# Kernel optimization log

Hardware: AMD Instinct MI355X
Metric: run time of the kernel (lower is better)

## Reference

```python
import jax, jax.numpy as jnp
import numpy as np

SCORE_THRESH = 0.5
NMS_THRESH = 0.4
TOP_K = 1000  # fixed pre-NMS candidate budget (jit-safe replacement for boolean masking)
STRIDES = (8, 16, 32)
H, W = 2176, 3840


def _anchor_centers(fh, fw, stride):
    yv, xv = jnp.meshgrid(jnp.arange(fh), jnp.arange(fw), indexing='ij')
    return (jnp.stack([xv, yv], -1).reshape(-1, 2).astype(jnp.float32)) * stride  # [N,2]


def _decode_level(scores, bbox, kps, stride):
    fh, fw = H // stride, W // stride
    c = _anchor_centers(fh, fw, stride)                 # [N,2]
    s = jax.nn.sigmoid(scores.reshape(-1))              # [N]
    d = bbox.reshape(-1, 4) * stride                    # [N,4]
    boxes = jnp.concatenate([c - d[:, :2], c + d[:, 2:4]], axis=1)  # x1y1x2y2
    k = kps.reshape(-1, 5, 2) * stride + c[:, None, :]  # (x,y) pairs
    return s, boxes, k.reshape(-1, 10)


def _iou_matrix(b):
    area = (b[:, 2] - b[:, 0]) * (b[:, 3] - b[:, 1])
    lt = jnp.maximum(b[:, None, :2], b[None, :, :2])
    rb = jnp.minimum(b[:, None, 2:], b[None, :, 2:])
    wh = jnp.clip(rb - lt, 0.0)
    inter = wh[..., 0] * wh[..., 1]
    return inter / jnp.clip(area[:, None] + area[None, :] - inter, 1e-9)


def _nms_keep(iou, valid):
    n = iou.shape[0]
    ar = jnp.arange(n)

    def body(i, keep):
        sup = (iou[i] > NMS_THRESH) & (ar > i) & keep[i]
        return keep & ~sup

    return jax.lax.fori_loop(0, n, body, valid)


def reference(x, scores8, bbox8, kps8, scores16, bbox16, kps16, scores32, bbox32, kps32):
    levels = ((scores8, bbox8, kps8), (scores16, bbox16, kps16), (scores32, bbox32, kps32))
    ss, bs, ks = [], [], []
    for (s, b, k), stride in zip(levels, STRIDES):
        si, bi, ki = _decode_level(s, b, k, stride)
        ss.append(si); bs.append(bi); ks.append(ki)
    scores = jnp.concatenate(ss)   # [N_total]
    boxes = jnp.concatenate(bs)    # [N_total,4]
    kpss = jnp.concatenate(ks)     # [N_total,10]

    masked = jnp.where(scores > SCORE_THRESH, scores, -1.0)
    top_s, idx = jax.lax.top_k(masked, TOP_K)
    valid = top_s > SCORE_THRESH
    b = boxes[idx]
    k = kpss[idx]

    keep = jax.lax.stop_gradient(_nms_keep(_iou_matrix(b), valid))
    final_boxes = jnp.where(keep[:, None], b, 0.0)
    final_scores = jnp.where(keep, top_s, 0.0)
    final_kpss = jnp.where(keep[:, None], k, 0.0)
    return final_boxes, final_scores, final_kpss


def setup_inputs() -> dict:
    key = jax.random.key(0)
    ks = jax.random.split(key, 10)
    n8 = (H // 8) * (W // 8)
    n16 = (H // 16) * (W // 16)
    n32 = (H // 32) * (W // 32)
    return {
        'x': jax.random.normal(ks[0], (1, 3, H, W), jnp.float32),
        'scores8': jax.random.normal(ks[1], (1, n8, 1), jnp.float32),
        'bbox8': jax.random.uniform(ks[2], (1, n8, 4), jnp.float32),
        'kps8': jax.random.normal(ks[3], (1, n8, 10), jnp.float32),
        'scores16': jax.random.normal(ks[4], (1, n16, 1), jnp.float32),
        'bbox16': jax.random.uniform(ks[5], (1, n16, 4), jnp.float32),
        'kps16': jax.random.normal(ks[6], (1, n16, 10), jnp.float32),
        'scores32': jax.random.normal(ks[7], (1, n32, 1), jnp.float32),
        'bbox32': jax.random.uniform(ks[8], (1, n32, 4), jnp.float32),
        'kps32': jax.random.normal(ks[9], (1, n32, 10), jnp.float32),
    }
```

## Files before the change

### kernel.cpp

```cpp
#include <hip/hip_runtime.h>
#include <stdint.h>

typedef unsigned int u32;
typedef unsigned long long u64;

#define N8   130560
#define N16  32640
#define N32  8160
#define NTOT 171360
#define NTOT4 42840
#define TOPK 1000
#define NWORDS 16
#define NBINS 4096
#define NREP 4
#define BUCKET_SCALE 682.0f
#define LIST_CAP 2048
#define NBLK 168
#define IOU_TASKS (TOPK * NWORDS)
#define IOU_BLKS 63
#define NMS_CACHE 256

#define OFF_HIST 0
#define OFF_META 65536
#define OFF_NZ   65792
#define MEMSET_BYTES 65920
#define OFF_LIST 65920
#define OFF_MASK 82304

__device__ __forceinline__ u64 ald64(const u64* p) {
  return __hip_atomic_load(p, __ATOMIC_RELAXED, __HIP_MEMORY_SCOPE_AGENT);
}
__device__ __forceinline__ void ast64(u64* p, u64 v) {
  __hip_atomic_store(p, v, __ATOMIC_RELAXED, __HIP_MEMORY_SCOPE_AGENT);
}

__device__ __forceinline__ u32 bucket_of(float x) {
  u32 b = (u32)(x * BUCKET_SCALE);
  return b > (NBINS - 1) ? (NBINS - 1) : b;
}

__device__ __forceinline__ float4 load_logit4(int v, const float* s8, const float* s16,
                                              const float* s32) {
  int e = v * 4;
  if (e < N8) return ((const float4*)s8)[v];
  if (e < N8 + N16) return ((const float4*)s16)[v - N8 / 4];
  return ((const float4*)s32)[v - (N8 + N16) / 4];
}

__device__ __forceinline__ bool iou_gt04(float4 a, float4 b) {
#pragma clang fp contract(off)
  float areaA = (a.z - a.x) * (a.w - a.y);
  float areaB = (b.z - b.x) * (b.w - b.y);
  float ltx = fmaxf(a.x, b.x);
  float lty = fmaxf(a.y, b.y);
  float rbx = fminf(a.z, b.z);
  float rby = fminf(a.w, b.w);
  float wx = rbx - ltx; wx = wx > 0.0f ? wx : 0.0f;
  float wy = rby - lty; wy = wy > 0.0f ? wy : 0.0f;
  float inter = wx * wy;
  float un = areaA + areaB - inter;
  un = un > 1e-9f ? un : 1e-9f;
  return (inter / un) > 0.4f;
}

__device__ __forceinline__ u64 valid_word(int w, u32 vcnt) {
  int lo = w * 64;
  if ((int)vcnt >= lo + 64) return ~0ull;
  if ((int)vcnt <= lo) return 0ull;
  return (1ull << (vcnt - (u32)lo)) - 1ull;
}

__global__ void __launch_bounds__(256) k_hist(
    const float* __restrict__ s8, const float* __restrict__ s16, const float* __restrict__ s32,
    u32* __restrict__ hist) {
  int v = blockIdx.x * 256 + threadIdx.x;
  if (v >= NTOT4) return;
  u32* h = hist + (blockIdx.x & (NREP - 1)) * NBINS;
  float4 x = load_logit4(v, s8, s16, s32);
  if (x.x > 0.0f) atomicAdd(&h[bucket_of(x.x)], 1u);
  if (x.y > 0.0f) atomicAdd(&h[bucket_of(x.y)], 1u);
  if (x.z > 0.0f) atomicAdd(&h[bucket_of(x.z)], 1u);
  if (x.w > 0.0f) atomicAdd(&h[bucket_of(x.w)], 1u);
}

__global__ void __launch_bounds__(256) k_findB_compact(
    const float* __restrict__ s8, const float* __restrict__ s16, const float* __restrict__ s32,
    const u32* __restrict__ hist, u32* __restrict__ meta, u64* __restrict__ list) {
  __shared__ u32 hloc[NBINS];
  __shared__ u32 csum[256];
  __shared__ u32 sB;
  int t = threadIdx.x;
#pragma unroll
  for (int k = 0; k < 16; ++k) {
    int b = k * 256 + t;
    u32 v = 0;
#pragma unroll
    for (int r = 0; r < NREP; ++r) v += hist[r * NBINS + b];
    hloc[b] = v;
  }
  __syncthreads();
  u32 sum = 0;
  int base = t * 16;
#pragma unroll
  for (int k = 0; k < 16; ++k) sum += hloc[base + k];
  csum[t] = sum;
  __syncthreads();
  for (int off = 1; off < 256; off <<= 1) {
    u32 add = (t + off < 256) ? csum[t + off] : 0u;
    __syncthreads();
    csum[t] += add;
    __syncthreads();
  }
  if (t == 0 && csum[0] < TOPK) sB = 0;
  u32 above = (t < 255) ? csum[t + 1] : 0u;
  if (csum[t] >= TOPK && above < TOPK) {
    u32 cum = above, Bv = (u32)(t * 16);
    for (int b = t * 16 + 15; b >= t * 16; --b) {
      cum += hloc[b];
      if (cum >= TOPK) { Bv = (u32)b; break; }
    }
    sB = Bv;
  }
  __syncthreads();
  const u32 B = sB;

  int v = blockIdx.x * 256 + t;
  if (v >= NTOT4) return;
  float4 x = load_logit4(v, s8, s16, s32);
  float c[4] = {x.x, x.y, x.z, x.w};
#pragma unroll
  for (int j = 0; j < 4; ++j) {
    float xx = c[j];
    if (xx > 0.0f && bucket_of(xx) >= B) {
      u32 pos = atomicAdd(&meta[1], 1u);
      if (pos < LIST_CAP) {
        u32 idx = (u32)(v * 4 + j);
        list[pos] = ((u64)__float_as_uint(xx) << 32) | (u64)(~idx);
      }
    }
  }
}

__global__ void __launch_bounds__(256) k_rank_decode(
    const u64* __restrict__ list, const u32* __restrict__ meta,
    const float* __restrict__ bb8,  const float* __restrict__ kp8,
    const float* __restrict__ bb16, const float* __restrict__ kp16,
    const float* __restrict__ bb32, const float* __restrict__ kp32,
    float* __restrict__ out) {
  __shared__ u64 keys[LIST_CAP];
  int t = threadIdx.x;
  u32 cnt = meta[1];
  if (cnt > LIST_CAP) cnt = LIST_CAP;
  for (int j = t; j < LIST_CAP; j += 256) keys[j] = (j < (int)cnt) ? list[j] : 0ull;
  __syncthreads();
  int tid = blockIdx.x * 256 + t;
  if (tid < (int)cnt) {
    u64 my = keys[tid];
    int rank = 0, j = 0;
    for (; j + 4 <= (int)cnt; j += 4)
      rank += (keys[j] > my) + (keys[j + 1] > my) + (keys[j + 2] > my) + (keys[j + 3] > my);
    for (; j < (int)cnt; ++j) rank += (keys[j] > my);
    if (rank < TOPK) {
      float lx = __uint_as_float((u32)(my >> 32));
      float sc = (float)(1.0 / (1.0 + exp(-(double)lx)));
      u32 idx = ~((u32)my);
      float4 box;
      float kv[10];
      int p, xq, yq;
      float st;
      const float *bb, *kp;
      if (idx < N8) {
        st = 8.f;  p = (int)idx;              xq = p % 480; yq = p / 480; bb = bb8;  kp = kp8;
      } else if (idx < N8 + N16) {
        st = 16.f; p = (int)idx - N8;         xq = p % 240; yq = p / 240; bb = bb16; kp = kp16;
      } else {
        st = 32.f; p = (int)idx - (N8 + N16); xq = p % 120; yq = p / 120; bb = bb32; kp = kp32;
      }
      float cx = (float)xq * st, cy = (float)yq * st;
      {
#pragma clang fp contract(off)
        float d0 = bb[4 * p + 0] * st;
        float d1 = bb[4 * p + 1] * st;
        float d2 = bb[4 * p + 2] * st;
        float d3 = bb[4 * p + 3] * st;
        box.x = cx - d0; box.y = cy - d1; box.z = cx + d2; box.w = cy + d3;
        for (int q = 0; q < 10; ++q)
          kv[q] = kp[10 * p + q] * st + ((q & 1) ? cy : cx);
      }
      ((float4*)out)[rank] = box;
      out[4000 + rank] = sc;
      for (int q = 0; q < 10; ++q) out[5000 + 10 * rank + q] = kv[q];
    }
  } else if (tid < TOPK) {
    ((float4*)out)[tid] = make_float4(0.f, 0.f, 0.f, 0.f);
    out[4000 + tid] = 0.f;
    for (int q = 0; q < 10; ++q) out[5000 + 10 * tid + q] = 0.f;
  }
}

__global__ void __launch_bounds__(256) k_iou_nms(
    const u32* __restrict__ meta_ro, u32* meta, u64* nzWords, u64* mask, float* out) {
  __shared__ __align__(16) char smem[36864];
  __shared__ int isLast;
  __shared__ u32 sPc[16], sOff17[17];
  __shared__ u64 sRem[NWORDS];
  int t = threadIdx.x;
  int blk = blockIdx.x;

  float4* boxes = (float4*)smem;
  for (int r = t; r < TOPK; r += 256) boxes[r] = ((const float4*)out)[r];
  __syncthreads();
  int task = blk * 256 + t;
  if (task < IOU_TASKS) {
    int w = task / 1000;
    int i = task - w * 1000;
    float4 a = boxes[i];
    int bse = w * 64;
    int jend = (bse + 64) < TOPK ? (bse + 64) : TOPK;
    u64 bits = 0;
    for (int j = bse; j < jend; ++j)
      if (j > i && iou_gt04(a, boxes[j])) bits |= 1ull << (j - bse);
    ast64(&mask[(u64)w * 1000 + i], bits);
    if (bits) atomicOr(&nzWords[i >> 6], 1ull << (i & 63));
  }
  __syncthreads();
  if (t == 0)
    isLast = (__hip_atomic_fetch_add(&meta[56], 1u, __ATOMIC_RELAXED,
                                     __HIP_MEMORY_SCOPE_AGENT) == (u32)(IOU_BLKS - 1));
  __syncthreads();
  if (!isLast) return;

  u32 cnt = meta_ro[1];
  if (cnt > LIST_CAP) cnt = LIST_CAP;
  const u32 vcnt = cnt < TOPK ? cnt : TOPK;
  u32* rows = (u32*)smem;
  u64* cache = (u64*)(smem + 4096);
  u64 nzv = 0;
  if (t < NWORDS) {
    nzv = ald64(&nzWords[t]) & valid_word(t, vcnt);
    sPc[t] = (u32)__popcll(nzv);
  }
  __syncthreads();
  if (t == 0) {
    u32 o = 0;
    for (int w = 0; w < NWORDS; ++w) { sOff17[w] = o; o += sPc[w]; }
    sOff17[16] = o;
  }
  __syncthreads();
  if (t < NWORDS) {
    u64 m = nzv;
    u32 o = sOff17[t];
    while (m) { int b = __builtin_ctzll(m); m &= m - 1; rows[o++] = (u32)(t * 64 + b); }
  }
  __syncthreads();
  const int S = (int)sOff17[16];
  const int Sc = S < NMS_CACHE ? S : NMS_CACHE;
  for (int idx = t; idx < Sc * NWORDS; idx += 256) {
    int s = idx >> 4, w = idx & 15;
    cache[s * NWORDS + w] = ald64(&mask[(u64)w * 1000 + rows[s]]);
  }
  __syncthreads();
  if (t < 64) {
    u64 remv = 0;
    for (int s = 0; s < S; ++s) {
      u32 row = rows[s];
      int c = (int)(row >> 6), b = (int)(row & 63);
      u64 remc = __shfl(remv, c);
      if (!((remc >> b) & 1ull)) {
        u64 m = 0;
        if (t < NWORDS)
          m = (s < NMS_CACHE) ? cache[s * NWORDS + t] : ald64(&mask[(u64)t * 1000 + row]);
        remv |= m;
      }
    }
    if (t < NWORDS) sRem[t] = valid_word(t, vcnt) & remv;
  }
  __syncthreads();
  for (int r = t; r < TOPK; r += 256) {
    if ((sRem[r >> 6] >> (r & 63)) & 1ull) {
      ((float4*)out)[r] = make_float4(0.f, 0.f, 0.f, 0.f);
      out[4000 + r] = 0.f;
      for (int q = 0; q < 10; ++q) out[5000 + 10 * r + q] = 0.f;
    }
  }
}

extern "C" void kernel_launch(void* const* d_in, const int* in_sizes, int n_in,
                              void* d_out, int out_size, void* d_ws, size_t ws_size,
                              hipStream_t stream) {
  const float* s8   = (const float*)d_in[1];
  const float* bb8  = (const float*)d_in[2];
  const float* kp8  = (const float*)d_in[3];
  const float* s16  = (const float*)d_in[4];
  const float* bb16 = (const float*)d_in[5];
  const float* kp16 = (const float*)d_in[6];
  const float* s32  = (const float*)d_in[7];
  const float* bb32 = (const float*)d_in[8];
  const float* kp32 = (const float*)d_in[9];

  char* ws = (char*)d_ws;
  u32* hist    = (u32*)(ws + OFF_HIST);
  u32* meta    = (u32*)(ws + OFF_META);
  u64* nzWords = (u64*)(ws + OFF_NZ);
  u64* list    = (u64*)(ws + OFF_LIST);
  u64* mask    = (u64*)(ws + OFF_MASK);
  float* out   = (float*)d_out;

  hipMemsetAsync(ws, 0, MEMSET_BYTES, stream);
  k_hist<<<NBLK, 256, 0, stream>>>(s8, s16, s32, hist);
  k_findB_compact<<<NBLK, 256, 0, stream>>>(s8, s16, s32, hist, meta, list);
  k_rank_decode<<<8, 256, 0, stream>>>(list, meta, bb8, kp8, bb16, kp16, bb32, kp32, out);
  k_iou_nms<<<IOU_BLKS, 256, 0, stream>>>(meta, meta, nzWords, mask, out);
}
```

Baseline: 205.5 us.

## Fuse threshold search, compaction and rank-decode into one kernel with grid-level spin sync

Removes the memset and merges the bin-threshold search, candidate compaction and rank/decode stages into a single kernel. Blocks coordinate through global atomic counters and spin-waits. The histogram now uses per-block shared-memory atomics and writes per-block partials, which are reduced in parallel across 32 blocks. Rank/decode is spread over 32 blocks of 64 active threads instead of 8 blocks. The aim is to cut launch and memset overhead and global atomic contention. In exchange it relies on all 168 blocks being co-resident and adds a larger partial-histogram write and read.

```diff
diff --git a/kernel.cpp b/kernel.cpp
--- a/kernel.cpp
+++ b/kernel.cpp
@@ -12,23 +12,30 @@
 #define TOPK 1000
 #define NWORDS 16
 #define NBINS 4096
-#define NREP 4
 #define BUCKET_SCALE 682.0f
 #define LIST_CAP 2048
 #define NBLK 168
+#define NRED 32
+#define RANK_BLKS 32
 #define IOU_TASKS (TOPK * NWORDS)
 #define IOU_BLKS 63
 #define NMS_CACHE 256
 
-#define OFF_HIST 0
-#define OFF_META 65536
-#define OFF_NZ   65792
-#define MEMSET_BYTES 65920
-#define OFF_LIST 65920
-#define OFF_MASK 82304
-
+#define OFF_PART 0
+#define OFF_RED  2752512
+#define OFF_META 2768896
+#define OFF_NZ   2769152
+#define OFF_LIST 2769280
+#define OFF_MASK 2785664
+
+__device__ __forceinline__ u32 ald32(const u32* p) {
+  return __hip_atomic_load(p, __ATOMIC_RELAXED, __HIP_MEMORY_SCOPE_AGENT);
+}
 __device__ __forceinline__ u64 ald64(const u64* p) {
   return __hip_atomic_load(p, __ATOMIC_RELAXED, __HIP_MEMORY_SCOPE_AGENT);
+}
+__device__ __forceinline__ void ast32(u32* p, u32 v) {
+  __hip_atomic_store(p, v, __ATOMIC_RELAXED, __HIP_MEMORY_SCOPE_AGENT);
 }
 __device__ __forceinline__ void ast64(u64* p, u64 v) {
   __hip_atomic_store(p, v, __ATOMIC_RELAXED, __HIP_MEMORY_SCOPE_AGENT);
@@ -72,88 +79,130 @@
 
 __global__ void __launch_bounds__(256) k_hist(
     const float* __restrict__ s8, const float* __restrict__ s16, const float* __restrict__ s32,
-    u32* __restrict__ hist) {
-  int v = blockIdx.x * 256 + threadIdx.x;
-  if (v >= NTOT4) return;
-  u32* h = hist + (blockIdx.x & (NREP - 1)) * NBINS;
-  float4 x = load_logit4(v, s8, s16, s32);
-  if (x.x > 0.0f) atomicAdd(&h[bucket_of(x.x)], 1u);
-  if (x.y > 0.0f) atomicAdd(&h[bucket_of(x.y)], 1u);
-  if (x.z > 0.0f) atomicAdd(&h[bucket_of(x.z)], 1u);
-  if (x.w > 0.0f) atomicAdd(&h[bucket_of(x.w)], 1u);
-}
-
-__global__ void __launch_bounds__(256) k_findB_compact(
+    u32* __restrict__ part, u32* __restrict__ meta, u64* __restrict__ nzWords) {
+  __shared__ u32 lh[NBINS];
+  int t = threadIdx.x, blk = blockIdx.x;
+#pragma unroll
+  for (int k = 0; k < 16; ++k) lh[k * 256 + t] = 0;
+  __syncthreads();
+  int v = blk * 256 + t;
+  if (v < NTOT4) {
+    float4 x = load_logit4(v, s8, s16, s32);
+    if (x.x > 0.0f) atomicAdd(&lh[bucket_of(x.x)], 1u);
+    if (x.y > 0.0f) atomicAdd(&lh[bucket_of(x.y)], 1u);
+    if (x.z > 0.0f) atomicAdd(&lh[bucket_of(x.z)], 1u);
+    if (x.w > 0.0f) atomicAdd(&lh[bucket_of(x.w)], 1u);
+  }
+  __syncthreads();
+#pragma unroll
+  for (int k = 0; k < 16; ++k) part[blk * NBINS + k * 256 + t] = lh[k * 256 + t];
+  if (blk == 0) {
+    if (t < 64) meta[t] = 0;
+    if (t < NWORDS) nzWords[t] = 0ull;
+  }
+}
+
+__global__ void __launch_bounds__(256) k_sel(
     const float* __restrict__ s8, const float* __restrict__ s16, const float* __restrict__ s32,
-    const u32* __restrict__ hist, u32* __restrict__ meta, u64* __restrict__ list) {
-  __shared__ u32 hloc[NBINS];
-  __shared__ u32 csum[256];
-  __shared__ u32 sB;
-  int t = threadIdx.x;
-#pragma unroll
-  for (int k = 0; k < 16; ++k) {
-    int b = k * 256 + t;
-    u32 v = 0;
-#pragma unroll
-    for (int r = 0; r < NREP; ++r) v += hist[r * NBINS + b];
-    hloc[b] = v;
-  }
-  __syncthreads();
-  u32 sum = 0;
-  int base = t * 16;
-#pragma unroll
-  for (int k = 0; k < 16; ++k) sum += hloc[base + k];
-  csum[t] = sum;
-  __syncthreads();
-  for (int off = 1; off < 256; off <<= 1) {
-    u32 add = (t + off < 256) ? csum[t + off] : 0u;
-    __syncthreads();
-    csum[t] += add;
-    __syncthreads();
-  }
-  if (t == 0 && csum[0] < TOPK) sB = 0;
-  u32 above = (t < 255) ? csum[t + 1] : 0u;
-  if (csum[t] >= TOPK && above < TOPK) {
-    u32 cum = above, Bv = (u32)(t * 16);
-    for (int b = t * 16 + 15; b >= t * 16; --b) {
-      cum += hloc[b];
-      if (cum >= TOPK) { Bv = (u32)b; break; }
-    }
-    sB = Bv;
-  }
-  __syncthreads();
-  const u32 B = sB;
-
-  int v = blockIdx.x * 256 + t;
-  if (v >= NTOT4) return;
-  float4 x = load_logit4(v, s8, s16, s32);
-  float c[4] = {x.x, x.y, x.z, x.w};
-#pragma unroll
-  for (int j = 0; j < 4; ++j) {
-    float xx = c[j];
-    if (xx > 0.0f && bucket_of(xx) >= B) {
-      u32 pos = atomicAdd(&meta[1], 1u);
-      if (pos < LIST_CAP) {
-        u32 idx = (u32)(v * 4 + j);
-        list[pos] = ((u64)__float_as_uint(xx) << 32) | (u64)(~idx);
-      }
-    }
-  }
-}
-
-__global__ void __launch_bounds__(256) k_rank_decode(
-    const u64* __restrict__ list, const u32* __restrict__ meta,
     const float* __restrict__ bb8,  const float* __restrict__ kp8,
     const float* __restrict__ bb16, const float* __restrict__ kp16,
     const float* __restrict__ bb32, const float* __restrict__ kp32,
+    const u32* __restrict__ part, u32* red, u32* meta, u64* list,
     float* __restrict__ out) {
-  __shared__ u64 keys[LIST_CAP];
-  int t = threadIdx.x;
-  u32 cnt = meta[1];
+  __shared__ __align__(16) char smem[16896];
+  __shared__ u32 sB, sCnt;
+  const int t = threadIdx.x, blk = blockIdx.x;
+  const int v = blk * 256 + t;
+
+  float4 x = make_float4(-1.f, -1.f, -1.f, -1.f);
+  if (v < NTOT4) x = load_logit4(v, s8, s16, s32);
+
+  if (blk < NRED) {
+    u32* lhs = (u32*)smem;
+    int bin = blk * 128 + (t & 127);
+    int pp = t >> 7;
+    u32 acc = 0;
+    for (int p = pp; p < NBLK; p += 2) acc += part[p * NBINS + bin];
+    lhs[t] = acc;
+    __syncthreads();
+    if (t < 128) ast32(&red[blk * 128 + t], lhs[t] + lhs[t + 128]);
+    __syncthreads();
+    if (t == 0)
+      __hip_atomic_fetch_add(&meta[3], 1u, __ATOMIC_RELAXED, __HIP_MEMORY_SCOPE_AGENT);
+  }
+
+  if (blk == 0) {
+    if (t == 0)
+      while (ald32(&meta[3]) < (u32)NRED) __builtin_amdgcn_s_sleep(2);
+    __syncthreads();
+    u32* hloc = (u32*)smem;
+    u32* csum = (u32*)(smem + 16384);
+#pragma unroll
+    for (int k = 0; k < 16; ++k) hloc[k * 256 + t] = ald32(&red[k * 256 + t]);
+    __syncthreads();
+    u32 sum = 0;
+    int base = t * 16;
+#pragma unroll
+    for (int k = 0; k < 16; ++k) sum += hloc[base + k];
+    csum[t] = sum;
+    __syncthreads();
+    for (int off = 1; off < 256; off <<= 1) {
+      u32 add = (t + off < 256) ? csum[t + off] : 0u;
+      __syncthreads();
+      csum[t] += add;
+      __syncthreads();
+    }
+    u32 above = (t < 255) ? csum[t + 1] : 0u;
+    if (t == 0 && csum[0] < TOPK) ast32(&meta[0], 0xC0DE0000u);
+    if (csum[t] >= TOPK && above < TOPK) {
+      u32 cum = above, Bv = (u32)(t * 16);
+      for (int b = t * 16 + 15; b >= t * 16; --b) {
+        cum += hloc[b];
+        if (cum >= TOPK) { Bv = (u32)b; break; }
+      }
+      ast32(&meta[0], 0xC0DE0000u | Bv);
+    }
+    __syncthreads();
+  }
+
+  if (t == 0) {
+    u32 pv;
+    while (((pv = ald32(&meta[0])) >> 16) != 0xC0DEu) __builtin_amdgcn_s_sleep(2);
+    sB = pv & 0xFFFFu;
+  }
+  __syncthreads();
+  const u32 B = sB;
+  if (v < NTOT4) {
+    float c[4] = {x.x, x.y, x.z, x.w};
+#pragma unroll
+    for (int j = 0; j < 4; ++j) {
+      float xx = c[j];
+      if (xx > 0.0f && bucket_of(xx) >= B) {
+        u32 pos = atomicAdd(&meta[1], 1u);
+        if (pos < LIST_CAP) {
+          u32 idx = (u32)(v * 4 + j);
+          ast64(&list[pos], ((u64)__float_as_uint(xx) << 32) | (u64)(~idx));
+        }
+      }
+    }
+  }
+  __syncthreads();
+  if (t == 0)
+    __hip_atomic_fetch_add(&meta[2], 1u, __ATOMIC_RELAXED, __HIP_MEMORY_SCOPE_AGENT);
+  if (blk >= RANK_BLKS) return;
+
+  if (t == 0) {
+    while (ald32(&meta[2]) < (u32)NBLK) __builtin_amdgcn_s_sleep(2);
+    sCnt = ald32(&meta[1]);
+  }
+  __syncthreads();
+  u32 cnt = sCnt;
   if (cnt > LIST_CAP) cnt = LIST_CAP;
-  for (int j = t; j < LIST_CAP; j += 256) keys[j] = (j < (int)cnt) ? list[j] : 0ull;
-  __syncthreads();
-  int tid = blockIdx.x * 256 + t;
+  u64* keys = (u64*)smem;
+  for (int j = t; j < LIST_CAP; j += 256) keys[j] = (j < (int)cnt) ? ald64(&list[j]) : 0ull;
+  __syncthreads();
+  if (t >= 64) return;
+  int tid = blk * 64 + t;
   if (tid < (int)cnt) {
     u64 my = keys[tid];
     int rank = 0, j = 0;
@@ -299,16 +348,16 @@
   const float* kp32 = (const float*)d_in[9];
 
   char* ws = (char*)d_ws;
-  u32* hist    = (u32*)(ws + OFF_HIST);
+  u32* part    = (u32*)(ws + OFF_PART);
+  u32* red     = (u32*)(ws + OFF_RED);
   u32* meta    = (u32*)(ws + OFF_META);
   u64* nzWords = (u64*)(ws + OFF_NZ);
   u64* list    = (u64*)(ws + OFF_LIST);
   u64* mask    = (u64*)(ws + OFF_MASK);
   float* out   = (float*)d_out;
 
-  hipMemsetAsync(ws, 0, MEMSET_BYTES, stream);
-  k_hist<<<NBLK, 256, 0, stream>>>(s8, s16, s32, hist);
-  k_findB_compact<<<NBLK, 256, 0, stream>>>(s8, s16, s32, hist, meta, list);
-  k_rank_decode<<<8, 256, 0, stream>>>(list, meta, bb8, kp8, bb16, kp16, bb32, kp32, out);
+  k_hist<<<NBLK, 256, 0, stream>>>(s8, s16, s32, part, meta, nzWords);
+  k_sel<<<NBLK, 256, 0, stream>>>(s8, s16, s32, bb8, kp8, bb16, kp16, bb32, kp32,
+                                  part, red, meta, list, out);
   k_iou_nms<<<IOU_BLKS, 256, 0, stream>>>(meta, meta, nzWords, mask, out);
 }
```

Result: slower. 211.9 us (+3.1%).
